# Performance work log

Measured on AMD Instinct MI355X. Metric: run time of the kernel, lower is better.

## Reference

```python
import jax, jax.numpy as jnp
import numpy as np

B, L, D, N, V = 32, 4096, 128, 5, 128  # batch, seq, embed dim, n-gram order, alphabet size


def setup_inputs() -> dict:
    key = jax.random.key(0)
    k1, k2, k3 = jax.random.split(key, 3)
    x = jax.random.randint(k1, (B, L), 0, V, dtype=jnp.int32)
    emb = jax.random.normal(k2, (V, D), dtype=jnp.float32)
    W = jax.random.normal(k3, (V, D * (N - 1)), dtype=jnp.float32) * 0.05
    b = jnp.zeros((V,), dtype=jnp.float32)
    return {"x": x, "emb": emb, "W": W, "b": b}


def reference(x, emb, W, b):
    n1 = N - 1  # context window size
    x_enc = emb[x]  # (B, L, D) embedding gather
    # enc[:, j, k*D:(k+1)*D] = x_enc[:, j - n1 + k] for j >= n1; zeros for j < n1.
    # Build each slot by right-shifting the embedded sequence by (n1 - k).
    Lcur = x.shape[1]
    parts = [jnp.pad(x_enc, ((0, 0), (n1 - k, 0), (0, 0)))[:, :Lcur] for k in range(n1)]
    enc = jnp.concatenate(parts, axis=-1)  # (B, L, n1*D)
    valid = (jnp.arange(Lcur) >= n1)[None, :, None]
    enc = jnp.where(valid, enc, jnp.zeros((), enc.dtype))
    # linear: logits = enc @ W^T + b  -> (B, L, V)
    logits = jnp.einsum("blf,vf->blv", enc, W) + b
    return logits
```

## Files before the change

### kernel.cpp

```cpp
#include <hip/hip_runtime.h>

constexpr int Bn = 32;
constexpr int Ln = 4096;
constexpr int Dn = 128;
constexpr int Vn = 128;
constexpr int N1 = 4;

__global__ void build_table_kernel(const float* __restrict__ emb,
                                   const float* __restrict__ W,
                                   float* __restrict__ T) {
    const int kt = blockIdx.x;
    const int k  = kt >> 7;
    const int t  = kt & 127;
    const int v  = threadIdx.x;

    __shared__ float4 e[Dn / 4];
    if (threadIdx.x < Dn / 4) {
        e[threadIdx.x] = ((const float4*)(emb + t * Dn))[threadIdx.x];
    }
    __syncthreads();

    const float4* w = (const float4*)(W + (size_t)v * (Dn * N1) + k * Dn);
    float acc = 0.f;
#pragma unroll
    for (int i = 0; i < Dn / 4; ++i) {
        float4 wv = w[i];
        float4 ev = e[i];
        acc += wv.x * ev.x + wv.y * ev.y + wv.z * ev.z + wv.w * ev.w;
    }
    T[(size_t)kt * Vn + v] = acc;
}

__global__ void ngram_logits_kernel(const int* __restrict__ x,
                                    const float* __restrict__ T,
                                    const float* __restrict__ bias,
                                    float* __restrict__ out) {
    const int tid = blockIdx.x * blockDim.x + threadIdx.x;
    const int vq  = tid & 31;
    const int pos = tid >> 5;
    const int j   = pos & (Ln - 1);

    float4 acc = ((const float4*)bias)[vq];

    if (j >= N1) {
        const int* xp = x + (pos - N1);
        const int t0 = xp[0];
        const int t1 = xp[1];
        const int t2 = xp[2];
        const int t3 = xp[3];
        const float4* Tq = (const float4*)T;
        const float4 a0 = Tq[(size_t)(0 * Vn + t0) * 32 + vq];
        const float4 a1 = Tq[(size_t)(1 * Vn + t1) * 32 + vq];
        const float4 a2 = Tq[(size_t)(2 * Vn + t2) * 32 + vq];
        const float4 a3 = Tq[(size_t)(3 * Vn + t3) * 32 + vq];
        acc.x += a0.x + a1.x + a2.x + a3.x;
        acc.y += a0.y + a1.y + a2.y + a3.y;
        acc.z += a0.z + a1.z + a2.z + a3.z;
        acc.w += a0.w + a1.w + a2.w + a3.w;
    }

    ((float4*)out)[(size_t)pos * 32 + vq] = acc;
}

extern "C" void kernel_launch(void* const* d_in, const int* in_sizes, int n_in,
                              void* d_out, int out_size, void* d_ws, size_t ws_size,
                              hipStream_t stream) {
    const int*   x    = (const int*)d_in[0];
    const float* emb  = (const float*)d_in[1];
    const float* W    = (const float*)d_in[2];
    const float* bias = (const float*)d_in[3];
    float*       out  = (float*)d_out;
    float*       T    = (float*)d_ws;

    build_table_kernel<<<N1 * Vn, Vn, 0, stream>>>(emb, W, T);

    const int total_threads = Bn * Ln * (Vn / 4);
    const int block = 256;
    ngram_logits_kernel<<<total_threads / block, block, 0, stream>>>(x, T, bias, out);
}
```

Before: 94.04 us.

## Fold bias into table, process four positions per thread, use nontemporal stores

Bias is added into the k=0 slice of the lookup table, so the logits kernel no longer loads or adds it per position. Each thread now handles four consecutive positions, loading the token window with two int4 reads and reusing it across positions, and writes the output with nontemporal stores. This aims to cut index-load traffic and thread count, and to keep the large output stream from polluting the cache. The cost is fewer threads with more registers each. The first four positions of each sequence still store the bias alone.

New measurement: 92.52 us (median of 2 runs). No clear change (-1.6%).

```diff
diff --git a/kernel.cpp b/kernel.cpp
--- a/kernel.cpp
+++ b/kernel.cpp
@@ -6,8 +6,11 @@
 constexpr int Vn = 128;
 constexpr int N1 = 4;
 
+typedef float vfloat4 __attribute__((ext_vector_type(4)));
+
 __global__ void build_table_kernel(const float* __restrict__ emb,
                                    const float* __restrict__ W,
+                                   const float* __restrict__ bias,
                                    float* __restrict__ T) {
     const int kt = blockIdx.x;
     const int k  = kt >> 7;
@@ -21,7 +24,7 @@
     __syncthreads();
 
     const float4* w = (const float4*)(W + (size_t)v * (Dn * N1) + k * Dn);
-    float acc = 0.f;
+    float acc = (k == 0) ? bias[v] : 0.f;
 #pragma unroll
     for (int i = 0; i < Dn / 4; ++i) {
         float4 wv = w[i];
@@ -31,35 +34,46 @@
     T[(size_t)kt * Vn + v] = acc;
 }
 
-__global__ void ngram_logits_kernel(const int* __restrict__ x,
-                                    const float* __restrict__ T,
-                                    const float* __restrict__ bias,
-                                    float* __restrict__ out) {
-    const int tid = blockIdx.x * blockDim.x + threadIdx.x;
-    const int vq  = tid & 31;
-    const int pos = tid >> 5;
-    const int j   = pos & (Ln - 1);
+__global__ void __launch_bounds__(256)
+ngram_logits_kernel(const int* __restrict__ x,
+                    const float* __restrict__ T,
+                    const float* __restrict__ bias,
+                    float* __restrict__ out) {
+    const int tid     = blockIdx.x * blockDim.x + threadIdx.x;
+    const int vq      = tid & 31;
+    const int g       = tid >> 5;
+    const int basepos = g << 2;
+    const int j0      = basepos & (Ln - 1);
 
-    float4 acc = ((const float4*)bias)[vq];
+    vfloat4* outq = (vfloat4*)out;
 
-    if (j >= N1) {
-        const int* xp = x + (pos - N1);
-        const int t0 = xp[0];
-        const int t1 = xp[1];
-        const int t2 = xp[2];
-        const int t3 = xp[3];
-        const float4* Tq = (const float4*)T;
-        const float4 a0 = Tq[(size_t)(0 * Vn + t0) * 32 + vq];
-        const float4 a1 = Tq[(size_t)(1 * Vn + t1) * 32 + vq];
-        const float4 a2 = Tq[(size_t)(2 * Vn + t2) * 32 + vq];
-        const float4 a3 = Tq[(size_t)(3 * Vn + t3) * 32 + vq];
-        acc.x += a0.x + a1.x + a2.x + a3.x;
-        acc.y += a0.y + a1.y + a2.y + a3.y;
-        acc.z += a0.z + a1.z + a2.z + a3.z;
-        acc.w += a0.w + a1.w + a2.w + a3.w;
+    if (j0 == 0) {
+        const vfloat4 bv = ((const vfloat4*)bias)[vq];
+#pragma unroll
+        for (int i = 0; i < 4; ++i)
+            __builtin_nontemporal_store(bv, &outq[(size_t)(basepos + i) * 32 + vq]);
+        return;
     }
 
-    ((float4*)out)[(size_t)pos * 32 + vq] = acc;
+    const int4 xa = *(const int4*)(x + basepos - 4);
+    const int4 xb = *(const int4*)(x + basepos);
+    int w[7] = {xa.x, xa.y, xa.z, xa.w, xb.x, xb.y, xb.z};
+
+    const vfloat4* Tq = (const vfloat4*)T;
+    vfloat4 acc[4];
+#pragma unroll
+    for (int i = 0; i < 4; ++i) {
+        vfloat4 a = Tq[(size_t)(0 * Vn + w[i + 0]) * 32 + vq];
+#pragma unroll
+        for (int k = 1; k < N1; ++k) {
+            a += Tq[(size_t)(k * Vn + w[i + k]) * 32 + vq];
+        }
+        acc[i] = a;
+    }
+
+#pragma unroll
+    for (int i = 0; i < 4; ++i)
+        __builtin_nontemporal_store(acc[i], &outq[(size_t)(basepos + i) * 32 + vq]);
 }
 
 extern "C" void kernel_launch(void* const* d_in, const int* in_sizes, int n_in,
@@ -72,9 +86,9 @@
     float*       out  = (float*)d_out;
     float*       T    = (float*)d_ws;
 
-    build_table_kernel<<<N1 * Vn, Vn, 0, stream>>>(emb, W, T);
+    build_table_kernel<<<N1 * Vn, Vn, 0, stream>>>(emb, W, bias, T);
 
-    const int total_threads = Bn * Ln * (Vn / 4);
+    const int total_threads = (Bn * Ln / 4) * (Vn / 4);
     const int block = 256;
     ngram_logits_kernel<<<total_threads / block, block, 0, stream>>>(x, T, bias, out);
 }
```
